# Kernel optimization log

Measured on AMD Instinct MI355X. Metric: run time of the kernel, lower is better.

## Reference

```python
import jax, jax.numpy as jnp
import numpy as np

N_NODES = 100000
IN_CH = 128
HID = 16
N_EDGES = 3200000


def setup_inputs() -> dict:
    key = jax.random.key(0)
    k1, k2, k3, k4 = jax.random.split(key, 4)
    x = jax.random.normal(k1, (N_NODES, IN_CH), dtype=jnp.float32)
    edge_index = jax.random.randint(k2, (2, N_EDGES), 0, N_NODES, dtype=jnp.int64)
    s1 = 1.0 / np.sqrt(IN_CH)
    s2 = 1.0 / np.sqrt(HID)
    W1 = jax.random.uniform(k3, (IN_CH, HID), dtype=jnp.float32, minval=-s1, maxval=s1)
    b1 = jnp.zeros((HID,), dtype=jnp.float32)
    W2 = jax.random.uniform(k4, (HID, HID), dtype=jnp.float32, minval=-s2, maxval=s2)
    b2 = jnp.zeros((HID,), dtype=jnp.float32)
    return {"x": x, "edge_index": edge_index, "W1": W1, "b1": b1, "W2": W2, "b2": b2}


def _gcn_layer(h, W, b, row, col, norm, n_nodes):
    # GCNConv: transform first (small hidden dim), then normalized sum aggregation
    h = h @ W  # [N, out]
    msg = h[row] * norm[:, None]  # gather over edges incl. self-loops
    out = jax.ops.segment_sum(msg, col, num_segments=n_nodes)
    return out + b


def reference(x, edge_index, W1, b1, W2, b2):
    n = x.shape[0]
    row, col = edge_index[0], edge_index[1]
    # add self-loops (PyG GCNConv default)
    loop = jnp.arange(n, dtype=edge_index.dtype)
    row_l = jnp.concatenate([row, loop])
    col_l = jnp.concatenate([col, loop])
    # symmetric normalization D^-1/2 (A+I) D^-1/2 (degree from target index)
    deg = jax.ops.segment_sum(jnp.ones_like(col_l, dtype=x.dtype), col_l, num_segments=n)
    dinv = jnp.where(deg > 0, jax.lax.rsqrt(deg), 0.0)
    norm = dinv[row_l] * dinv[col_l]

    h = _gcn_layer(x, W1, b1, row_l, col_l, norm, n)
    h = jax.nn.relu(h)  # dropout is identity at eval
    h = _gcn_layer(h, W2, b2, row_l, col_l, norm, n)

    # fused per-edge dot-product link score + sigmoid (original edges only)
    scores = jnp.sum(h[row] * h[col], axis=-1)
    return jax.nn.sigmoid(scores)
```

## Files before the change

kernel.cpp:

```cpp
#include <hip/hip_runtime.h>
#include <hip/hip_bf16.h>
#include <hip/hip_fp16.h>
#include <math.h>


#define BSH 9
#define BSZ 512
#define PA_BLOCKS 256

__global__ __launch_bounds__(512) void pA(const int* __restrict__ col,
                                          int* __restrict__ M, int E, int CH, int NBUK) {
    extern __shared__ int hist[];
    const int t = threadIdx.x, b = blockIdx.x;
    for (int i = t; i < NBUK; i += 512) hist[i] = 0;
    __syncthreads();
    const int s = b * CH, e = min(E, s + CH);
    for (int i = s + t; i < e; i += 512) atomicAdd(&hist[col[i] >> BSH], 1);
    __syncthreads();
    for (int i = t; i < NBUK; i += 512) M[b * NBUK + i] = hist[i];
}

__global__ __launch_bounds__(256) void pB1(int* __restrict__ M, int* __restrict__ T, int NBUK) {
    __shared__ int s[256];
    const int t = threadIdx.x, k = blockIdx.x;
    int own = M[t * NBUK + k];
    s[t] = own;
    __syncthreads();
    for (int d = 1; d < 256; d <<= 1) {
        int add = (t >= d) ? s[t - d] : 0;
        __syncthreads();
        s[t] += add;
        __syncthreads();
    }
    M[t * NBUK + k] = s[t] - own;
    if (t == 255) T[k] = s[255];
}

__global__ __launch_bounds__(256) void pB2(const int* __restrict__ T, int* __restrict__ S, int NBUK) {
    __shared__ int s[256];
    const int t = threadIdx.x;
    int own = (t < NBUK) ? T[t] : 0;
    s[t] = own;
    __syncthreads();
    for (int d = 1; d < 256; d <<= 1) {
        int add = (t >= d) ? s[t - d] : 0;
        __syncthreads();
        s[t] += add;
        __syncthreads();
    }
    if (t < NBUK) S[t] = s[t] - own;
    if (t == 255) S[NBUK] = s[255];
}

__global__ __launch_bounds__(512) void pC(const int* __restrict__ row, const int* __restrict__ col,
                                          const int* __restrict__ M, const int* __restrict__ S,
                                          unsigned int* __restrict__ ebuf, int E, int CH, int NBUK) {
    extern __shared__ int cur[];
    const int t = threadIdx.x, b = blockIdx.x;
    for (int i = t; i < NBUK; i += 512) cur[i] = S[i] + M[b * NBUK + i];
    __syncthreads();
    const int s = b * CH, e = min(E, s + CH);
    for (int i = s + t; i < e; i += 512) {
        int c = col[i], r = row[i];
        int p = atomicAdd(&cur[c >> BSH], 1);
        ebuf[p] = ((unsigned int)(c & (BSZ - 1)) << 17) | (unsigned int)r;
    }
}

__global__ __launch_bounds__(512) void pC2(const unsigned int* __restrict__ ebuf,
                                           const int* __restrict__ S,
                                           unsigned int* __restrict__ ebuf2,
                                           float* __restrict__ dinv,
                                           int* __restrict__ start, int N) {
    __shared__ int h[BSZ], sc[BSZ], cur[BSZ];
    const int t = threadIdx.x, k = blockIdx.x;
    h[t] = 0;
    __syncthreads();
    const int s = S[k], e = S[k + 1];
    for (int i = s + t; i < e; i += 512) atomicAdd(&h[ebuf[i] >> 17], 1);
    __syncthreads();
    sc[t] = h[t];
    __syncthreads();
    for (int d = 1; d < 512; d <<= 1) {
        int add = (t >= d) ? sc[t - d] : 0;
        __syncthreads();
        sc[t] += add;
        __syncthreads();
    }
    cur[t] = sc[t] - h[t];
    const int v = (k << BSH) + t;
    if (v < N) {
        dinv[v] = rsqrtf((float)h[t] + 1.0f);
        start[v] = s + cur[t];
    }
    __syncthreads();
    for (int i = s + t; i < e; i += 512) {
        unsigned int w = ebuf[i];
        int p = atomicAdd(&cur[w >> 17], 1);
        ebuf2[s + p] = w;
    }
}

__global__ void kTail(int* __restrict__ start, int N, int E) { start[N] = E; }

__global__ __launch_bounds__(256) void k_gemm1(
    const float* __restrict__ x, const float* __restrict__ W1,
    const float* __restrict__ dinv, __half* __restrict__ ts, int N) {
    __shared__ float wsT[16 * 132];
    const int tid = threadIdx.x;
    for (int idx = tid; idx < 2048; idx += 256) {
        int k = idx >> 4, c = idx & 15;
        wsT[c * 132 + k] = W1[idx];
    }
    __syncthreads();
    const int n = blockIdx.x * 256 + tid;
    if (n >= N) return;
    const float4* xr = (const float4*)(x + (size_t)n * 128);
    float acc[16];
    #pragma unroll
    for (int c = 0; c < 16; ++c) acc[c] = 0.f;
    #pragma unroll 4
    for (int k4 = 0; k4 < 32; ++k4) {
        float4 a = xr[k4];
        #pragma unroll
        for (int c = 0; c < 16; ++c) {
            const float4 w = *(const float4*)&wsT[c * 132 + k4 * 4];
            acc[c] = fmaf(a.x, w.x, fmaf(a.y, w.y, fmaf(a.z, w.z, fmaf(a.w, w.w, acc[c]))));
        }
    }
    float dv = dinv[n];
    union { __half h[16]; uint4 u[2]; } o;
    #pragma unroll
    for (int c = 0; c < 16; ++c) o.h[c] = __float2half(acc[c] * dv);
    uint4* dst = (uint4*)(ts + (size_t)n * 16);
    dst[0] = o.u[0]; dst[1] = o.u[1];
}

__global__ __launch_bounds__(256) void pGat1(
    const unsigned int* __restrict__ ebuf2, const int* __restrict__ start,
    const __half* __restrict__ ts1h, const float* __restrict__ dinv,
    const float* __restrict__ b1, const float* __restrict__ W2,
    __half* __restrict__ ts2h, int N) {
    __shared__ float w2s[256];
    const int tid = threadIdx.x;
    w2s[tid] = W2[tid];
    __syncthreads();
    const int lane = tid & 15;
    const int v = blockIdx.x * 16 + (tid >> 4);
    if (v >= N) return;
    const int s = start[v], e = start[v + 1];
    float sum = 0.f;
    int i = s;
    for (; i + 4 <= e; i += 4) {
        int r0 = ebuf2[i]     & 0x1FFFF;
        int r1 = ebuf2[i + 1] & 0x1FFFF;
        int r2 = ebuf2[i + 2] & 0x1FFFF;
        int r3 = ebuf2[i + 3] & 0x1FFFF;
        float v0 = __half2float(ts1h[(size_t)r0 * 16 + lane]);
        float v1 = __half2float(ts1h[(size_t)r1 * 16 + lane]);
        float v2 = __half2float(ts1h[(size_t)r2 * 16 + lane]);
        float v3 = __half2float(ts1h[(size_t)r3 * 16 + lane]);
        sum += (v0 + v1) + (v2 + v3);
    }
    for (; i < e; ++i) {
        int r = ebuf2[i] & 0x1FFFF;
        sum += __half2float(ts1h[(size_t)r * 16 + lane]);
    }
    float dv = dinv[v];
    float h = fmaxf(dv * (sum + __half2float(ts1h[(size_t)v * 16 + lane])) + b1[lane], 0.f);
    float o = 0.f;
    #pragma unroll
    for (int j = 0; j < 16; ++j)
        o = fmaf(__shfl(h, j, 16), w2s[j * 16 + lane], o);
    ts2h[(size_t)v * 16 + lane] = __float2half(dv * o);
}

__global__ __launch_bounds__(256) void pGat2(
    const unsigned int* __restrict__ ebuf2, const int* __restrict__ start,
    const __half* __restrict__ ts2h, const float* __restrict__ dinv,
    const float* __restrict__ b2, __half* __restrict__ h2h, int N) {
    const int tid = threadIdx.x;
    const int lane = tid & 15;
    const int v = blockIdx.x * 16 + (tid >> 4);
    if (v >= N) return;
    const int s = start[v], e = start[v + 1];
    float sum = 0.f;
    int i = s;
    for (; i + 4 <= e; i += 4) {
        int r0 = ebuf2[i]     & 0x1FFFF;
        int r1 = ebuf2[i + 1] & 0x1FFFF;
        int r2 = ebuf2[i + 2] & 0x1FFFF;
        int r3 = ebuf2[i + 3] & 0x1FFFF;
        float v0 = __half2float(ts2h[(size_t)r0 * 16 + lane]);
        float v1 = __half2float(ts2h[(size_t)r1 * 16 + lane]);
        float v2 = __half2float(ts2h[(size_t)r2 * 16 + lane]);
        float v3 = __half2float(ts2h[(size_t)r3 * 16 + lane]);
        sum += (v0 + v1) + (v2 + v3);
    }
    for (; i < e; ++i) {
        int r = ebuf2[i] & 0x1FFFF;
        sum += __half2float(ts2h[(size_t)r * 16 + lane]);
    }
    float a = sum + __half2float(ts2h[(size_t)v * 16 + lane]);
    h2h[(size_t)v * 16 + lane] = __float2half(dinv[v] * a + b2[lane]);
}

__global__ void k_score(const int* __restrict__ row, const int* __restrict__ col,
                        const __half* __restrict__ h2h, float* __restrict__ out, int E) {
    int e = blockIdx.x * 256 + threadIdx.x;
    if (e < E) {
        union { uint4 u[2]; __half2 h[8]; } a, b;
        const uint4* pa = (const uint4*)(h2h + (size_t)row[e] * 16);
        const uint4* pb = (const uint4*)(h2h + (size_t)col[e] * 16);
        a.u[0] = pa[0]; a.u[1] = pa[1];
        b.u[0] = pb[0]; b.u[1] = pb[1];
        float d = 0.f;
        #pragma unroll
        for (int i = 0; i < 8; ++i) {
            float2 fa = __half22float2(a.h[i]);
            float2 fb = __half22float2(b.h[i]);
            d = fmaf(fa.x, fb.x, fmaf(fa.y, fb.y, d));
        }
        out[e] = 1.0f / (1.0f + __expf(-d));
    }
}

__global__ void k_countf(const int* __restrict__ col, float* __restrict__ deg, int E) {
    int e = blockIdx.x * 256 + threadIdx.x;
    if (e < E) atomicAdd(&deg[col[e]], 1.0f);
}
__global__ void k_dinvf(float* __restrict__ dinv, int N) {
    int v = blockIdx.x * 256 + threadIdx.x;
    if (v < N) dinv[v] = rsqrtf(dinv[v] + 1.0f);
}
__global__ __launch_bounds__(256) void k_gemm1f(
    const float* __restrict__ x, const float* __restrict__ W1,
    const float* __restrict__ dinv, float* __restrict__ ts, int N) {
    __shared__ float wsT[16 * 132];
    const int tid = threadIdx.x;
    for (int idx = tid; idx < 2048; idx += 256) {
        int k = idx >> 4, c = idx & 15;
        wsT[c * 132 + k] = W1[idx];
    }
    __syncthreads();
    const int n = blockIdx.x * 256 + tid;
    if (n >= N) return;
    const float4* xr = (const float4*)(x + (size_t)n * 128);
    float acc[16];
    #pragma unroll
    for (int c = 0; c < 16; ++c) acc[c] = 0.f;
    for (int k4 = 0; k4 < 32; ++k4) {
        float4 a = xr[k4];
        #pragma unroll
        for (int c = 0; c < 16; ++c) {
            const float4 w = *(const float4*)&wsT[c * 132 + k4 * 4];
            acc[c] = fmaf(a.x, w.x, fmaf(a.y, w.y, fmaf(a.z, w.z, fmaf(a.w, w.w, acc[c]))));
        }
    }
    float dv = dinv[n];
    float4* o = (float4*)(ts + (size_t)n * 16);
    #pragma unroll
    for (int q = 0; q < 4; ++q)
        o[q] = make_float4(acc[4*q] * dv, acc[4*q+1] * dv, acc[4*q+2] * dv, acc[4*q+3] * dv);
}
__global__ void k_scatter(const int* __restrict__ row, const int* __restrict__ col,
                          const float* __restrict__ ts, float* __restrict__ acc, int E) {
    int g = blockIdx.x * 256 + threadIdx.x;
    int e = g >> 4, c = g & 15;
    if (e < E) atomicAdd(&acc[(size_t)col[e] * 16 + c], ts[(size_t)row[e] * 16 + c]);
}
__global__ void k_finalize(float* __restrict__ acc, const float* __restrict__ ts,
                           const float* __restrict__ dinv, const float* __restrict__ b,
                           int N, int relu) {
    int g = blockIdx.x * 256 + threadIdx.x;
    int v = g >> 4, c = g & 15;
    if (v < N) {
        float h = dinv[v] * (acc[g] + ts[g]) + b[c];
        if (relu) h = fmaxf(h, 0.f);
        acc[g] = h;
    }
}
__global__ __launch_bounds__(256) void k_gemm2f(
    const float* __restrict__ h1, const float* __restrict__ W2,
    const float* __restrict__ dinv, float* __restrict__ ts2, int N) {
    __shared__ float hs[16 * 17];
    __shared__ float ws2[256];
    const int tid = threadIdx.x;
    const int base = blockIdx.x * 16;
    if (tid < 64) ((float4*)ws2)[tid] = ((const float4*)W2)[tid];
    if (tid >= 64 && tid < 128) {
        int t2 = tid - 64;
        float4 v4 = ((const float4*)(h1 + (size_t)base * 16))[t2];
        float* d = &hs[(t2 >> 2) * 17 + (t2 & 3) * 4];
        d[0] = v4.x; d[1] = v4.y; d[2] = v4.z; d[3] = v4.w;
    }
    __syncthreads();
    const int r = tid >> 4, c = tid & 15;
    float a = 0.f;
    #pragma unroll
    for (int kk = 0; kk < 16; ++kk) a = fmaf(hs[r * 17 + kk], ws2[kk * 16 + c], a);
    ts2[(size_t)(base + r) * 16 + c] = a * dinv[base + r];
}
__global__ void k_scoref(const int* __restrict__ row, const int* __restrict__ col,
                         const float* __restrict__ h2, float* __restrict__ out, int E) {
    int e = blockIdx.x * 256 + threadIdx.x;
    if (e < E) {
        const float4* a = (const float4*)(h2 + (size_t)row[e] * 16);
        const float4* b = (const float4*)(h2 + (size_t)col[e] * 16);
        float d = 0.f;
        #pragma unroll
        for (int i = 0; i < 4; ++i) {
            float4 u = a[i], v = b[i];
            d += u.x * v.x + u.y * v.y + u.z * v.z + u.w * v.w;
        }
        out[e] = 1.0f / (1.0f + __expf(-d));
    }
}

extern "C" void kernel_launch(void* const* d_in, const int* in_sizes, int n_in,
                              void* d_out, int out_size, void* d_ws, size_t ws_size,
                              hipStream_t stream) {
    const float* x  = (const float*)d_in[0];
    const int*   ei = (const int*)d_in[1];
    const float* W1 = (const float*)d_in[2];
    const float* b1 = (const float*)d_in[3];
    const float* W2 = (const float*)d_in[4];
    const float* b2 = (const float*)d_in[5];

    const int N = in_sizes[0] / 128;
    const int E = in_sizes[1] / 2;
    const int* row = ei;
    const int* col = ei + E;
    float* out = (float*)d_out;

    const int NBUK = (N + BSZ - 1) / BSZ;
    const int CH = (E + PA_BLOCKS - 1) / PA_BLOCKS;

    char* ws = (char*)d_ws;
    size_t off = 0;
    auto alloc = [&](size_t bytes) { void* p = ws + off; off += (bytes + 255) & ~(size_t)255; return p; };
    float*  dinv  = (float*)alloc((size_t)N * 4);
    __half* ts1h  = (__half*)alloc((size_t)N * 32);
    __half* ts2h  = (__half*)alloc((size_t)N * 32);
    int*    start = (int*)alloc((size_t)(N + 1) * 4);
    int*    M     = (int*)alloc((size_t)PA_BLOCKS * NBUK * 4);
    int*    T     = (int*)alloc((size_t)NBUK * 4);
    int*    S     = (int*)alloc((size_t)(NBUK + 1) * 4);
    unsigned int* ebuf  = (unsigned int*)alloc((size_t)E * 4);
    unsigned int* ebuf2 = (unsigned int*)alloc((size_t)E * 4);
    const size_t need = off;

    if (N <= 131072 && NBUK <= 256 && ws_size >= need) {
        const size_t ldsA = (size_t)NBUK * 4;
        pA <<<PA_BLOCKS, 512, ldsA, stream>>>(col, M, E, CH, NBUK);
        pB1<<<NBUK, 256, 0, stream>>>(M, T, NBUK);
        pB2<<<1, 256, 0, stream>>>(T, S, NBUK);
        pC <<<PA_BLOCKS, 512, ldsA, stream>>>(row, col, M, S, ebuf, E, CH, NBUK);
        pC2<<<NBUK, 512, 0, stream>>>(ebuf, S, ebuf2, dinv, start, N);
        kTail<<<1, 1, 0, stream>>>(start, N, E);
        k_gemm1<<<(N + 255) / 256, 256, 0, stream>>>(x, W1, dinv, ts1h, N);
        pGat1<<<(N + 15) / 16, 256, 0, stream>>>(ebuf2, start, ts1h, dinv, b1, W2, ts2h, N);
        __half* h2h = ts1h;
        pGat2<<<(N + 15) / 16, 256, 0, stream>>>(ebuf2, start, ts2h, dinv, b2, h2h, N);
        k_score<<<(E + 255) / 256, 256, 0, stream>>>(row, col, h2h, out, E);
    } else {
        float* dinvF = (float*)ws;
        float* ts1F  = (float*)(ws + (size_t)N * 4);
        float* ts2F  = (float*)(ws + (size_t)N * 4 + (size_t)N * 64);
        hipMemsetAsync(dinvF, 0, (size_t)N * 4, stream);
        hipMemsetAsync(ts2F, 0, (size_t)N * 64, stream);
        k_countf<<<(E + 255) / 256, 256, 0, stream>>>(col, dinvF, E);
        k_dinvf<<<(N + 255) / 256, 256, 0, stream>>>(dinvF, N);
        k_gemm1f<<<(N + 255) / 256, 256, 0, stream>>>(x, W1, dinvF, ts1F, N);
        k_scatter<<<(E * 16) / 256, 256, 0, stream>>>(row, col, ts1F, ts2F, E);
        k_finalize<<<(N * 16 + 255) / 256, 256, 0, stream>>>(ts2F, ts1F, dinvF, b1, N, 1);
        k_gemm2f<<<N / 16, 256, 0, stream>>>(ts2F, W2, dinvF, ts1F, N);
        hipMemsetAsync(ts2F, 0, (size_t)N * 64, stream);
        k_scatter<<<(E * 16) / 256, 256, 0, stream>>>(row, col, ts1F, ts2F, E);
        k_finalize<<<(N * 16 + 255) / 256, 256, 0, stream>>>(ts2F, ts1F, dinvF, b2, N, 0);
        k_scoref<<<(E + 255) / 256, 256, 0, stream>>>(row, col, ts2F, out, E);
    }
}
```

Baseline: 282.6 us.

## Halve bucket size, fold tail write into scan, gather half2 per lane in aggregation

Node buckets shrink from 512 to 256, so the CSR build uses about twice as many buckets: the top-level scan grows to 512 threads and pC2 runs 256-thread blocks, each with smaller per-bucket work. The standalone kernel that wrote start[N] is removed, and that write moves into the top-level scan, saving one launch. Both gather kernels now use 8 lanes per node, each loading a half2, so a block covers 32 nodes and makes half as many but wider loads. The trade-offs are larger per-block histogram matrices M in pA/pC and more shuffle-based matmul work per lane.

Result: no change. 283.5 us (+0.3%).

```diff
diff --git a/kernel.cpp b/kernel.cpp
--- a/kernel.cpp
+++ b/kernel.cpp
@@ -4,8 +4,8 @@
 #include <math.h>
 
 
-#define BSH 9
-#define BSZ 512
+#define BSH 8
+#define BSZ 256
 #define PA_BLOCKS 256
 
 __global__ __launch_bounds__(512) void pA(const int* __restrict__ col,
@@ -36,20 +36,22 @@
     if (t == 255) T[k] = s[255];
 }
 
-__global__ __launch_bounds__(256) void pB2(const int* __restrict__ T, int* __restrict__ S, int NBUK) {
-    __shared__ int s[256];
+__global__ __launch_bounds__(512) void pB2(const int* __restrict__ T, int* __restrict__ S,
+                                           int* __restrict__ start, int NBUK, int N, int E) {
+    __shared__ int s[512];
     const int t = threadIdx.x;
     int own = (t < NBUK) ? T[t] : 0;
     s[t] = own;
     __syncthreads();
-    for (int d = 1; d < 256; d <<= 1) {
+    for (int d = 1; d < 512; d <<= 1) {
         int add = (t >= d) ? s[t - d] : 0;
         __syncthreads();
         s[t] += add;
         __syncthreads();
     }
     if (t < NBUK) S[t] = s[t] - own;
-    if (t == 255) S[NBUK] = s[255];
+    if (t == 511) S[NBUK] = s[511];
+    if (t == 0) start[N] = E;
 }
 
 __global__ __launch_bounds__(512) void pC(const int* __restrict__ row, const int* __restrict__ col,
@@ -67,7 +69,7 @@
     }
 }
 
-__global__ __launch_bounds__(512) void pC2(const unsigned int* __restrict__ ebuf,
+__global__ __launch_bounds__(256) void pC2(const unsigned int* __restrict__ ebuf,
                                            const int* __restrict__ S,
                                            unsigned int* __restrict__ ebuf2,
                                            float* __restrict__ dinv,
@@ -77,11 +79,11 @@
     h[t] = 0;
     __syncthreads();
     const int s = S[k], e = S[k + 1];
-    for (int i = s + t; i < e; i += 512) atomicAdd(&h[ebuf[i] >> 17], 1);
+    for (int i = s + t; i < e; i += 256) atomicAdd(&h[ebuf[i] >> 17], 1);
     __syncthreads();
     sc[t] = h[t];
     __syncthreads();
-    for (int d = 1; d < 512; d <<= 1) {
+    for (int d = 1; d < 256; d <<= 1) {
         int add = (t >= d) ? sc[t - d] : 0;
         __syncthreads();
         sc[t] += add;
@@ -94,14 +96,12 @@
         start[v] = s + cur[t];
     }
     __syncthreads();
-    for (int i = s + t; i < e; i += 512) {
+    for (int i = s + t; i < e; i += 256) {
         unsigned int w = ebuf[i];
         int p = atomicAdd(&cur[w >> 17], 1);
         ebuf2[s + p] = w;
     }
 }
-
-__global__ void kTail(int* __restrict__ start, int N, int E) { start[N] = E; }
 
 __global__ __launch_bounds__(256) void k_gemm1(
     const float* __restrict__ x, const float* __restrict__ W1,
@@ -138,71 +138,84 @@
 
 __global__ __launch_bounds__(256) void pGat1(
     const unsigned int* __restrict__ ebuf2, const int* __restrict__ start,
-    const __half* __restrict__ ts1h, const float* __restrict__ dinv,
+    const __half2* __restrict__ tsv, const float* __restrict__ dinv,
     const float* __restrict__ b1, const float* __restrict__ W2,
-    __half* __restrict__ ts2h, int N) {
+    __half2* __restrict__ ts2v, int N) {
     __shared__ float w2s[256];
     const int tid = threadIdx.x;
     w2s[tid] = W2[tid];
     __syncthreads();
-    const int lane = tid & 15;
-    const int v = blockIdx.x * 16 + (tid >> 4);
+    const int l = tid & 7;
+    const int v = blockIdx.x * 32 + (tid >> 3);
     if (v >= N) return;
     const int s = start[v], e = start[v + 1];
-    float sum = 0.f;
+    float sx = 0.f, sy = 0.f;
     int i = s;
     for (; i + 4 <= e; i += 4) {
         int r0 = ebuf2[i]     & 0x1FFFF;
         int r1 = ebuf2[i + 1] & 0x1FFFF;
         int r2 = ebuf2[i + 2] & 0x1FFFF;
         int r3 = ebuf2[i + 3] & 0x1FFFF;
-        float v0 = __half2float(ts1h[(size_t)r0 * 16 + lane]);
-        float v1 = __half2float(ts1h[(size_t)r1 * 16 + lane]);
-        float v2 = __half2float(ts1h[(size_t)r2 * 16 + lane]);
-        float v3 = __half2float(ts1h[(size_t)r3 * 16 + lane]);
-        sum += (v0 + v1) + (v2 + v3);
+        float2 f0 = __half22float2(tsv[(size_t)r0 * 8 + l]);
+        float2 f1 = __half22float2(tsv[(size_t)r1 * 8 + l]);
+        float2 f2 = __half22float2(tsv[(size_t)r2 * 8 + l]);
+        float2 f3 = __half22float2(tsv[(size_t)r3 * 8 + l]);
+        sx += (f0.x + f1.x) + (f2.x + f3.x);
+        sy += (f0.y + f1.y) + (f2.y + f3.y);
     }
     for (; i < e; ++i) {
         int r = ebuf2[i] & 0x1FFFF;
-        sum += __half2float(ts1h[(size_t)r * 16 + lane]);
-    }
-    float dv = dinv[v];
-    float h = fmaxf(dv * (sum + __half2float(ts1h[(size_t)v * 16 + lane])) + b1[lane], 0.f);
-    float o = 0.f;
-    #pragma unroll
-    for (int j = 0; j < 16; ++j)
-        o = fmaf(__shfl(h, j, 16), w2s[j * 16 + lane], o);
-    ts2h[(size_t)v * 16 + lane] = __float2half(dv * o);
+        float2 f = __half22float2(tsv[(size_t)r * 8 + l]);
+        sx += f.x; sy += f.y;
+    }
+    const float dv = dinv[v];
+    float2 sf = __half22float2(tsv[(size_t)v * 8 + l]);
+    float hx = fmaxf(dv * (sx + sf.x) + b1[2 * l],     0.f);
+    float hy = fmaxf(dv * (sy + sf.y) + b1[2 * l + 1], 0.f);
+    float ox = 0.f, oy = 0.f;
+    #pragma unroll
+    for (int j = 0; j < 8; ++j) {
+        float ax = __shfl(hx, j, 8);
+        float ay = __shfl(hy, j, 8);
+        ox = fmaf(ax, w2s[(2 * j) * 16 + 2 * l],     fmaf(ay, w2s[(2 * j + 1) * 16 + 2 * l],     ox));
+        oy = fmaf(ax, w2s[(2 * j) * 16 + 2 * l + 1], fmaf(ay, w2s[(2 * j + 1) * 16 + 2 * l + 1], oy));
+    }
+    ts2v[(size_t)v * 8 + l] = __halves2half2(__float2half(dv * ox), __float2half(dv * oy));
 }
 
 __global__ __launch_bounds__(256) void pGat2(
     const unsigned int* __restrict__ ebuf2, const int* __restrict__ start,
-    const __half* __restrict__ ts2h, const float* __restrict__ dinv,
-    const float* __restrict__ b2, __half* __restrict__ h2h, int N) {
-    const int tid = threadIdx.x;
-    const int lane = tid & 15;
-    const int v = blockIdx.x * 16 + (tid >> 4);
+    const __half2* __restrict__ tsv, const float* __restrict__ dinv,
+    const float* __restrict__ b2, __half2* __restrict__ h2v, int N) {
+    const int tid = threadIdx.x;
+    const int l = tid & 7;
+    const int v = blockIdx.x * 32 + (tid >> 3);
     if (v >= N) return;
     const int s = start[v], e = start[v + 1];
-    float sum = 0.f;
+    float sx = 0.f, sy = 0.f;
     int i = s;
     for (; i + 4 <= e; i += 4) {
         int r0 = ebuf2[i]     & 0x1FFFF;
         int r1 = ebuf2[i + 1] & 0x1FFFF;
         int r2 = ebuf2[i + 2] & 0x1FFFF;
         int r3 = ebuf2[i + 3] & 0x1FFFF;
-        float v0 = __half2float(ts2h[(size_t)r0 * 16 + lane]);
-        float v1 = __half2float(ts2h[(size_t)r1 * 16 + lane]);
-        float v2 = __half2float(ts2h[(size_t)r2 * 16 + lane]);
-        float v3 = __half2float(ts2h[(size_t)r3 * 16 + lane]);
-        sum += (v0 + v1) + (v2 + v3);
+        float2 f0 = __half22float2(tsv[(size_t)r0 * 8 + l]);
+        float2 f1 = __half22float2(tsv[(size_t)r1 * 8 + l]);
+        float2 f2 = __half22float2(tsv[(size_t)r2 * 8 + l]);
+        float2 f3 = __half22float2(tsv[(size_t)r3 * 8 + l]);
+        sx += (f0.x + f1.x) + (f2.x + f3.x);
+        sy += (f0.y + f1.y) + (f2.y + f3.y);
     }
     for (; i < e; ++i) {
         int r = ebuf2[i] & 0x1FFFF;
-        sum += __half2float(ts2h[(size_t)r * 16 + lane]);
-    }
-    float a = sum + __half2float(ts2h[(size_t)v * 16 + lane]);
-    h2h[(size_t)v * 16 + lane] = __float2half(dinv[v] * a + b2[lane]);
+        float2 f = __half22float2(tsv[(size_t)r * 8 + l]);
+        sx += f.x; sy += f.y;
+    }
+    float2 sf = __half22float2(tsv[(size_t)v * 8 + l]);
+    const float dv = dinv[v];
+    h2v[(size_t)v * 8 + l] = __halves2half2(
+        __float2half(dv * (sx + sf.x) + b2[2 * l]),
+        __float2half(dv * (sy + sf.y) + b2[2 * l + 1]));
 }
 
 __global__ void k_score(const int* __restrict__ row, const int* __restrict__ col,
@@ -350,18 +363,19 @@
     unsigned int* ebuf2 = (unsigned int*)alloc((size_t)E * 4);
     const size_t need = off;
 
-    if (N <= 131072 && NBUK <= 256 && ws_size >= need) {
+    if (N <= 131072 && NBUK <= 512 && ws_size >= need) {
         const size_t ldsA = (size_t)NBUK * 4;
         pA <<<PA_BLOCKS, 512, ldsA, stream>>>(col, M, E, CH, NBUK);
         pB1<<<NBUK, 256, 0, stream>>>(M, T, NBUK);
-        pB2<<<1, 256, 0, stream>>>(T, S, NBUK);
+        pB2<<<1, 512, 0, stream>>>(T, S, start, NBUK, N, E);
         pC <<<PA_BLOCKS, 512, ldsA, stream>>>(row, col, M, S, ebuf, E, CH, NBUK);
-        pC2<<<NBUK, 512, 0, stream>>>(ebuf, S, ebuf2, dinv, start, N);
-        kTail<<<1, 1, 0, stream>>>(start, N, E);
+        pC2<<<NBUK, 256, 0, stream>>>(ebuf, S, ebuf2, dinv, start, N);
         k_gemm1<<<(N + 255) / 256, 256, 0, stream>>>(x, W1, dinv, ts1h, N);
-        pGat1<<<(N + 15) / 16, 256, 0, stream>>>(ebuf2, start, ts1h, dinv, b1, W2, ts2h, N);
+        pGat1<<<(N + 31) / 32, 256, 0, stream>>>(ebuf2, start, (const __half2*)ts1h, dinv, b1, W2,
+                                                 (__half2*)ts2h, N);
         __half* h2h = ts1h;
-        pGat2<<<(N + 15) / 16, 256, 0, stream>>>(ebuf2, start, ts2h, dinv, b2, h2h, N);
+        pGat2<<<(N + 31) / 32, 256, 0, stream>>>(ebuf2, start, (const __half2*)ts2h, dinv, b2,
+                                                 (__half2*)h2h, N);
         k_score<<<(E + 255) / 256, 256, 0, stream>>>(row, col, h2h, out, E);
     } else {
         float* dinvF = (float*)ws;
```
